# Performance work log

Measured on AMD Instinct MI355X. Metric: run time of the kernel, lower is better.

Reference implementation:

```python
import jax, jax.numpy as jnp
import numpy as np
import math

B, T, D, H, L = 64, 255, 512, 8, 8
CODEBOOK = 512
V = CODEBOOK + 3  # bos/eos/pad
COND_DIM = 512
MAX_LEN = 256
HD = D // H


def _layernorm(x, g, b, eps=1e-5):
    mu = jnp.mean(x, axis=-1, keepdims=True)
    var = jnp.mean(jnp.square(x - mu), axis=-1, keepdims=True)
    return (x - mu) * jax.lax.rsqrt(var + eps) * g + b


def setup_inputs() -> dict:
    key = jax.random.key(0)
    ks = jax.random.split(key, 24)
    s = 0.02
    d = {
        'tokens': jax.random.randint(ks[0], (B, T), 0, V),
        'cond': jax.random.normal(ks[1], (B, COND_DIM), jnp.float32),
        'emb': jax.random.normal(ks[2], (V, D), jnp.float32) * s,  # tied token_emb / head weight
        'pos_emb': jax.random.normal(ks[3], (1, MAX_LEN, D), jnp.float32) * s,
        'cond_w1': jax.random.normal(ks[4], (COND_DIM, D), jnp.float32) * s,
        'cond_b1': jnp.zeros((D,), jnp.float32),
        'cond_w2': jax.random.normal(ks[5], (D, D), jnp.float32) * s,
        'cond_b2': jnp.zeros((D,), jnp.float32),
        'ln1_g': jnp.ones((L, D), jnp.float32),
        'ln1_b': jnp.zeros((L, D), jnp.float32),
        'qkv_w': jax.random.normal(ks[6], (L, D, 3 * D), jnp.float32) * s,
        'qkv_b': jnp.zeros((L, 3 * D), jnp.float32),
        'proj_w': jax.random.normal(ks[7], (L, D, D), jnp.float32) * s,
        'proj_b': jnp.zeros((L, D), jnp.float32),
        'ln2_g': jnp.ones((L, D), jnp.float32),
        'ln2_b': jnp.zeros((L, D), jnp.float32),
        'mlp_w1': jax.random.normal(ks[8], (L, D, 4 * D), jnp.float32) * s,
        'mlp_b1': jnp.zeros((L, 4 * D), jnp.float32),
        'mlp_w2': jax.random.normal(ks[9], (L, 4 * D, D), jnp.float32) * s,
        'mlp_b2': jnp.zeros((L, D), jnp.float32),
        'lnf_g': jnp.ones((D,), jnp.float32),
        'lnf_b': jnp.zeros((D,), jnp.float32),
    }
    return d


def reference(tokens, cond, emb, pos_emb, cond_w1, cond_b1, cond_w2, cond_b2,
              ln1_g, ln1_b, qkv_w, qkv_b, proj_w, proj_b,
              ln2_g, ln2_b, mlp_w1, mlp_b1, mlp_w2, mlp_b2, lnf_g, lnf_b):
    b, t = tokens.shape
    h = emb[tokens] + pos_emb[:, :t, :]                              # [B,T,D]
    c = jax.nn.silu(cond @ cond_w1 + cond_b1) @ cond_w2 + cond_b2    # [B,D]
    h = jnp.concatenate([c[:, None, :], h], axis=1)                  # [B,S,D]
    S = t + 1
    causal = jnp.tril(jnp.ones((S, S), bool))
    scale = 1.0 / math.sqrt(HD)
    for i in range(L):
        x = _layernorm(h, ln1_g[i], ln1_b[i])
        qkv = (x @ qkv_w[i] + qkv_b[i]).reshape(b, S, 3, H, HD).transpose(2, 0, 3, 1, 4)
        q, k, v = qkv[0], qkv[1], qkv[2]                             # [B,H,S,hd]
        a = jnp.einsum('bhsd,bhtd->bhst', q, k) * scale
        a = jnp.where(causal, a, -jnp.inf)
        a = jax.nn.softmax(a, axis=-1)
        o = jnp.einsum('bhst,bhtd->bhsd', a, v).transpose(0, 2, 1, 3).reshape(b, S, D)
        h = h + o @ proj_w[i] + proj_b[i]
        x = _layernorm(h, ln2_g[i], ln2_b[i])
        h = h + jax.nn.gelu(x @ mlp_w1[i] + mlp_b1[i], approximate=False) @ mlp_w2[i] + mlp_b2[i]
    h = _layernorm(h, lnf_g, lnf_b)
    return (h @ emb.T)[:, 1:, :]                                     # [B,T,V]
```

## Files before the change

kernel.cpp:

```cpp
#include <hip/hip_runtime.h>
#include <hip/hip_bf16.h>

typedef __attribute__((ext_vector_type(8))) short bf16x8;
typedef __attribute__((ext_vector_type(4))) float f32x4;
typedef __attribute__((ext_vector_type(4))) unsigned short u16x4;
typedef __attribute__((ext_vector_type(8))) unsigned short u16x8;
typedef unsigned short u16;

#define DEV static __device__ __forceinline__

DEV float bf2f(u16 u) {
  union { unsigned int i; float f; } c; c.i = ((unsigned int)u) << 16; return c.f;
}
DEV u16 f2bf(float f) {
  union { float f; unsigned int i; } c; c.f = f;
  unsigned int i = c.i;
  i += 0x7FFFu + ((i >> 16) & 1u);
  return (u16)(i >> 16);
}

DEV void gload_lds16(const void* g, void* l) {
  __builtin_amdgcn_global_load_lds((const __attribute__((address_space(1))) void*)g,
                                   (__attribute__((address_space(3))) void*)l, 16, 0, 0);
}

DEV f32x4 mfma16(bf16x8 a, bf16x8 b, f32x4 c) {
  return __builtin_amdgcn_mfma_f32_16x16x32_bf16(a, b, c, 0, 0, 0);
}

__global__ __launch_bounds__(256) void ktranspose(const float* __restrict__ in, u16* __restrict__ out,
                                                  int K, int N) {
  __shared__ u16 tile[32][33];
  const float* src = in + (size_t)blockIdx.z * K * N;
  u16* dst = out + (size_t)blockIdx.z * K * N;
  const int n0 = blockIdx.x * 32, k0 = blockIdx.y * 32;
  const int tx = threadIdx.x, ty = threadIdx.y;
#pragma unroll
  for (int i = ty; i < 32; i += 8) tile[i][tx] = f2bf(src[(size_t)(k0 + i) * N + n0 + tx]);
  __syncthreads();
#pragma unroll
  for (int i = ty; i < 32; i += 8) dst[(size_t)(n0 + i) * K + k0 + tx] = tile[tx][i];
}

__global__ __launch_bounds__(256) void kcvt(const float* __restrict__ in, u16* __restrict__ out, int n) {
  int i = blockIdx.x * 256 + threadIdx.x;
  if (i < n) out[i] = f2bf(in[i]);
}

__global__ __launch_bounds__(256) void kcond(const float* __restrict__ cond, const float* __restrict__ w1,
                                             const float* __restrict__ b1, const float* __restrict__ w2,
                                             const float* __restrict__ b2, float* __restrict__ h) {
  __shared__ float xr[512];
  __shared__ float t1[512];
  const int b = blockIdx.x, tid = threadIdx.x;
  for (int i = tid; i < 512; i += 256) xr[i] = cond[b * 512 + i];
  __syncthreads();
  for (int j = tid; j < 512; j += 256) {
    float acc = b1[j];
    for (int k = 0; k < 512; ++k) acc += xr[k] * w1[k * 512 + j];
    t1[j] = acc / (1.f + __expf(-acc));
  }
  __syncthreads();
  for (int j = tid; j < 512; j += 256) {
    float acc = b2[j];
    for (int k = 0; k < 512; ++k) acc += t1[k] * w2[k * 512 + j];
    h[(size_t)b * 256 * 512 + j] = acc;
  }
}

__global__ __launch_bounds__(256) void kembed(const int* __restrict__ tok, const float* __restrict__ emb,
                                              const float* __restrict__ pos, float* __restrict__ h) {
  const int idx = blockIdx.x;
  const int b = idx / 255, t = idx % 255;
  const int c = threadIdx.x * 2;
  const int tk = tok[idx];
  float2 ev = *(const float2*)(emb + (size_t)tk * 512 + c);
  float2 pv = *(const float2*)(pos + (size_t)t * 512 + c);
  float2 r;
  r.x = ev.x + pv.x;
  r.y = ev.y + pv.y;
  *(float2*)(h + ((size_t)b * 256 + 1 + t) * 512 + c) = r;
}

__global__ __launch_bounds__(64) void kln(const float* __restrict__ hin, const float* __restrict__ g,
                                          const float* __restrict__ bt, u16* __restrict__ out) {
  const int row = blockIdx.x, lane = threadIdx.x;
  const float4* x = (const float4*)(hin + (size_t)row * 512);
  float4 v0 = x[lane], v1 = x[lane + 64];
  float s1 = v0.x + v0.y + v0.z + v0.w + v1.x + v1.y + v1.z + v1.w;
  float s2 = v0.x * v0.x + v0.y * v0.y + v0.z * v0.z + v0.w * v0.w +
             v1.x * v1.x + v1.y * v1.y + v1.z * v1.z + v1.w * v1.w;
#pragma unroll
  for (int off = 1; off < 64; off <<= 1) { s1 += __shfl_xor(s1, off); s2 += __shfl_xor(s2, off); }
  float mu = s1 * (1.f / 512.f);
  float var = s2 * (1.f / 512.f) - mu * mu;
  float rs = rsqrtf(var + 1e-5f);
  const int c0 = lane * 4;
  float4 g0 = *(const float4*)(g + c0), g1 = *(const float4*)(g + 256 + c0);
  float4 b0 = *(const float4*)(bt + c0), b1 = *(const float4*)(bt + 256 + c0);
  u16x4 o0, o1;
  o0[0] = f2bf((v0.x - mu) * rs * g0.x + b0.x);
  o0[1] = f2bf((v0.y - mu) * rs * g0.y + b0.y);
  o0[2] = f2bf((v0.z - mu) * rs * g0.z + b0.z);
  o0[3] = f2bf((v0.w - mu) * rs * g0.w + b0.w);
  o1[0] = f2bf((v1.x - mu) * rs * g1.x + b1.x);
  o1[1] = f2bf((v1.y - mu) * rs * g1.y + b1.y);
  o1[2] = f2bf((v1.z - mu) * rs * g1.z + b1.z);
  o1[3] = f2bf((v1.w - mu) * rs * g1.w + b1.w);
  *(u16x4*)(out + (size_t)row * 512 + c0) = o0;
  *(u16x4*)(out + (size_t)row * 512 + 256 + c0) = o1;
}

template<int MODE>
__global__ __launch_bounds__(256, 2) void kgemm(const u16* __restrict__ A, const u16* __restrict__ Bt,
                                                const float* __restrict__ bias, void* __restrict__ Cout,
                                                int M, int N, int K) {
  __shared__ __align__(16) u16 As[2][4096];
  __shared__ __align__(16) u16 Bs[2][4096];
  const int tid = threadIdx.x;
  const int lane = tid & 63;
  const int wr = tid >> 7, wc = (tid >> 6) & 1;
  const int m0 = blockIdx.x * 128, n0 = blockIdx.y * 128;
  const int nkt = K >> 5;
  const int Kb = K * 2;

  const int c0 = tid * 16;
  const int ar0 = c0 >> 6, ao0 = c0 & 63;
  const int ar1 = (c0 + 4096) >> 6, ao1 = (c0 + 4096) & 63;
  int br0 = n0 + ar0, br1 = n0 + ar1;
  if (MODE == 3) { br0 = min(br0, N - 1); br1 = min(br1, N - 1); }
  const char* Ab = (const char*)A;
  const char* Bb = (const char*)Bt;
  const size_t a0 = (size_t)(m0 + ar0) * Kb + ao0;
  const size_t a1 = (size_t)(m0 + ar1) * Kb + ao1;
  const size_t b0 = (size_t)br0 * Kb + ao0;
  const size_t b1 = (size_t)br1 * Kb + ao1;

  f32x4 acc[4][4];
#pragma unroll
  for (int i = 0; i < 4; ++i)
#pragma unroll
    for (int j = 0; j < 4; ++j) acc[i][j] = f32x4{0.f, 0.f, 0.f, 0.f};

  gload_lds16(Ab + a0, (char*)As[0] + c0);
  gload_lds16(Ab + a1, (char*)As[0] + c0 + 4096);
  gload_lds16(Bb + b0, (char*)Bs[0] + c0);
  gload_lds16(Bb + b1, (char*)Bs[0] + c0 + 4096);
  __syncthreads();

  const int aoff = (wr * 64 + (lane & 15)) * 32 + (lane >> 4) * 8;
  const int boff = (wc * 64 + (lane & 15)) * 32 + (lane >> 4) * 8;

  int buf = 0;
  for (int kt = 0; kt < nkt; ++kt) {
    if (kt + 1 < nkt) {
      const size_t ko = (size_t)(kt + 1) * 64;
      gload_lds16(Ab + a0 + ko, (char*)As[buf ^ 1] + c0);
      gload_lds16(Ab + a1 + ko, (char*)As[buf ^ 1] + c0 + 4096);
      gload_lds16(Bb + b0 + ko, (char*)Bs[buf ^ 1] + c0);
      gload_lds16(Bb + b1 + ko, (char*)Bs[buf ^ 1] + c0 + 4096);
    }
    bf16x8 aF[4], bF[4];
#pragma unroll
    for (int mt = 0; mt < 4; ++mt) aF[mt] = *(const bf16x8*)&As[buf][aoff + mt * 512];
#pragma unroll
    for (int nt = 0; nt < 4; ++nt) bF[nt] = *(const bf16x8*)&Bs[buf][boff + nt * 512];
#pragma unroll
    for (int mt = 0; mt < 4; ++mt)
#pragma unroll
      for (int nt = 0; nt < 4; ++nt)
        acc[mt][nt] = mfma16(aF[mt], bF[nt], acc[mt][nt]);
    __syncthreads();
    buf ^= 1;
  }

  float bv[4];
#pragma unroll
  for (int nt = 0; nt < 4; ++nt) {
    int col = n0 + wc * 64 + nt * 16 + (lane & 15);
    bv[nt] = (MODE == 3) ? 0.f : bias[col];
  }

  if (MODE == 0 || MODE == 1) {
    u16* C = (u16*)Cout;
#pragma unroll
    for (int mt = 0; mt < 4; ++mt)
#pragma unroll
      for (int r = 0; r < 4; ++r) {
        int row = m0 + wr * 64 + mt * 16 + (lane >> 4) * 4 + r;
        u16* cp = C + (size_t)row * N + n0 + wc * 64 + (lane & 15);
#pragma unroll
        for (int nt = 0; nt < 4; ++nt) {
          float v = acc[mt][nt][r] + bv[nt];
          if (MODE == 1) v = 0.5f * v * (1.f + erff(v * 0.70710678118f));
          cp[nt * 16] = f2bf(v);
        }
      }
  } else if (MODE == 2) {
    float* hC = (float*)Cout;
#pragma unroll
    for (int mt = 0; mt < 4; ++mt)
#pragma unroll
      for (int r = 0; r < 4; ++r) {
        int row = m0 + wr * 64 + mt * 16 + (lane >> 4) * 4 + r;
        float* hp = hC + (size_t)row * N + n0 + wc * 64 + (lane & 15);
#pragma unroll
        for (int nt = 0; nt < 4; ++nt) hp[nt * 16] += acc[mt][nt][r] + bv[nt];
      }
  } else {
    float* C = (float*)Cout;
#pragma unroll
    for (int mt = 0; mt < 4; ++mt)
#pragma unroll
      for (int r = 0; r < 4; ++r) {
        int row = m0 + wr * 64 + mt * 16 + (lane >> 4) * 4 + r;
        int s = row & 255;
        if (s == 0) continue;
        int bb = row >> 8;
        float* cp = C + ((size_t)bb * 255 + (s - 1)) * 515 + n0 + wc * 64 + (lane & 15);
#pragma unroll
        for (int nt = 0; nt < 4; ++nt) {
          int col = n0 + wc * 64 + nt * 16 + (lane & 15);
          if (col < 515) cp[nt * 16] = acc[mt][nt][r];
        }
      }
  }
}

__global__ __launch_bounds__(256, 1) void kattn(const u16* __restrict__ qkv, u16* __restrict__ o) {
  __shared__ __align__(16) u16 Ks[256][72];
  __shared__ __align__(16) u16 Vt[64][264];
  __shared__ __align__(16) u16 Ps[4][64][72];
  const int tid = threadIdx.x, wv = tid >> 6, lane = tid & 63;
  const int bh = blockIdx.x, bb = bh >> 3, hh = bh & 7;
  const size_t base = (size_t)bb * 256 * 1536 + hh * 64;

  for (int c = tid; c < 2048; c += 256) {
    int s = c >> 3, pp = c & 7;
    u16x8 kv = *(const u16x8*)(qkv + base + (size_t)s * 1536 + 512 + pp * 8);
    *(u16x8*)&Ks[s][pp * 8] = kv;
    u16x8 vv = *(const u16x8*)(qkv + base + (size_t)s * 1536 + 1024 + pp * 8);
#pragma unroll
    for (int j = 0; j < 8; ++j) Vt[pp * 8 + j][s] = vv[j];
  }
  __syncthreads();

  bf16x8 qf[4][2];
#pragma unroll
  for (int mt = 0; mt < 4; ++mt)
#pragma unroll
    for (int ks = 0; ks < 2; ++ks)
      qf[mt][ks] = *(const bf16x8*)(qkv + base +
                   (size_t)(wv * 64 + mt * 16 + (lane & 15)) * 1536 + ks * 32 + (lane >> 4) * 8);

  const float scale = 0.125f;
  float mrow[4][4], lsum[4][4];
#pragma unroll
  for (int mt = 0; mt < 4; ++mt)
#pragma unroll
    for (int r = 0; r < 4; ++r) { mrow[mt][r] = -1e30f; lsum[mt][r] = 0.f; }

  for (int ct = 0; ct <= wv; ++ct) {
    f32x4 sacc[4][4];
#pragma unroll
    for (int i = 0; i < 4; ++i)
#pragma unroll
      for (int j = 0; j < 4; ++j) sacc[i][j] = f32x4{0.f, 0.f, 0.f, 0.f};
#pragma unroll
    for (int ks = 0; ks < 2; ++ks) {
      bf16x8 kf[4];
#pragma unroll
      for (int nt = 0; nt < 4; ++nt)
        kf[nt] = *(const bf16x8*)&Ks[ct * 64 + nt * 16 + (lane & 15)][ks * 32 + (lane >> 4) * 8];
#pragma unroll
      for (int mt = 0; mt < 4; ++mt)
#pragma unroll
        for (int nt = 0; nt < 4; ++nt)
          sacc[mt][nt] = mfma16(qf[mt][ks], kf[nt], sacc[mt][nt]);
    }
#pragma unroll
    for (int mt = 0; mt < 4; ++mt)
#pragma unroll
      for (int r = 0; r < 4; ++r) {
        int srow = wv * 64 + mt * 16 + (lane >> 4) * 4 + r;
        float mx = -1e30f;
#pragma unroll
        for (int nt = 0; nt < 4; ++nt) {
          int tcol = ct * 64 + nt * 16 + (lane & 15);
          float v = sacc[mt][nt][r] * scale;
          if (tcol > srow) v = -1e30f;
          mx = fmaxf(mx, v);
        }
#pragma unroll
        for (int off = 1; off < 16; off <<= 1) mx = fmaxf(mx, __shfl_xor(mx, off));
        mrow[mt][r] = fmaxf(mrow[mt][r], mx);
      }
  }

  f32x4 oacc[4][4];
#pragma unroll
  for (int i = 0; i < 4; ++i)
#pragma unroll
    for (int j = 0; j < 4; ++j) oacc[i][j] = f32x4{0.f, 0.f, 0.f, 0.f};

  for (int ct = 0; ct <= wv; ++ct) {
    f32x4 sacc[4][4];
#pragma unroll
    for (int i = 0; i < 4; ++i)
#pragma unroll
      for (int j = 0; j < 4; ++j) sacc[i][j] = f32x4{0.f, 0.f, 0.f, 0.f};
#pragma unroll
    for (int ks = 0; ks < 2; ++ks) {
      bf16x8 kf[4];
#pragma unroll
      for (int nt = 0; nt < 4; ++nt)
        kf[nt] = *(const bf16x8*)&Ks[ct * 64 + nt * 16 + (lane & 15)][ks * 32 + (lane >> 4) * 8];
#pragma unroll
      for (int mt = 0; mt < 4; ++mt)
#pragma unroll
        for (int nt = 0; nt < 4; ++nt)
          sacc[mt][nt] = mfma16(qf[mt][ks], kf[nt], sacc[mt][nt]);
    }
#pragma unroll
    for (int mt = 0; mt < 4; ++mt)
#pragma unroll
      for (int r = 0; r < 4; ++r) {
        int srow = wv * 64 + mt * 16 + (lane >> 4) * 4 + r;
        float ps = 0.f;
#pragma unroll
        for (int nt = 0; nt < 4; ++nt) {
          int tcol = ct * 64 + nt * 16 + (lane & 15);
          float v = sacc[mt][nt][r] * scale;
          float pe = (tcol > srow) ? 0.f : __expf(v - mrow[mt][r]);
          ps += pe;
          Ps[wv][mt * 16 + (lane >> 4) * 4 + r][nt * 16 + (lane & 15)] = f2bf(pe);
        }
#pragma unroll
        for (int off = 1; off < 16; off <<= 1) ps += __shfl_xor(ps, off);
        lsum[mt][r] += ps;
      }
#pragma unroll
    for (int ks = 0; ks < 2; ++ks) {
      bf16x8 pf[4], vf[4];
#pragma unroll
      for (int mt = 0; mt < 4; ++mt)
        pf[mt] = *(const bf16x8*)&Ps[wv][mt * 16 + (lane & 15)][ks * 32 + (lane >> 4) * 8];
#pragma unroll
      for (int nt = 0; nt < 4; ++nt)
        vf[nt] = *(const bf16x8*)&Vt[nt * 16 + (lane & 15)][ct * 64 + ks * 32 + (lane >> 4) * 8];
#pragma unroll
      for (int mt = 0; mt < 4; ++mt)
#pragma unroll
        for (int nt = 0; nt < 4; ++nt)
          oacc[mt][nt] = mfma16(pf[mt], vf[nt], oacc[mt][nt]);
    }
  }

#pragma unroll
  for (int mt = 0; mt < 4; ++mt)
#pragma unroll
    for (int r = 0; r < 4; ++r) {
      int s = wv * 64 + mt * 16 + (lane >> 4) * 4 + r;
      float inv = 1.f / lsum[mt][r];
      u16* op = o + ((size_t)bb * 256 + s) * 512 + hh * 64 + (lane & 15);
#pragma unroll
      for (int nt = 0; nt < 4; ++nt) op[nt * 16] = f2bf(oacc[mt][nt][r] * inv);
    }
}

extern "C" void kernel_launch(void* const* d_in, const int* in_sizes, int n_in,
                              void* d_out, int out_size, void* d_ws, size_t ws_size,
                              hipStream_t stream) {
  const int* tokens = (const int*)d_in[0];
  const float* cond = (const float*)d_in[1];
  const float* emb = (const float*)d_in[2];
  const float* pos = (const float*)d_in[3];
  const float* cw1 = (const float*)d_in[4];
  const float* cb1 = (const float*)d_in[5];
  const float* cw2 = (const float*)d_in[6];
  const float* cb2 = (const float*)d_in[7];
  const float* ln1g = (const float*)d_in[8];
  const float* ln1b = (const float*)d_in[9];
  const float* qkvw = (const float*)d_in[10];
  const float* qkvb = (const float*)d_in[11];
  const float* projw = (const float*)d_in[12];
  const float* projb = (const float*)d_in[13];
  const float* ln2g = (const float*)d_in[14];
  const float* ln2b = (const float*)d_in[15];
  const float* w1 = (const float*)d_in[16];
  const float* b1 = (const float*)d_in[17];
  const float* w2 = (const float*)d_in[18];
  const float* b2 = (const float*)d_in[19];
  const float* lnfg = (const float*)d_in[20];
  const float* lnfb = (const float*)d_in[21];

  const size_t NEEDED = (size_t)16384 * 512 * 4
                      + (size_t)16384 * 512 * 2
                      + (size_t)16384 * 2048 * 2
                      + (size_t)8 * 1536 * 512 * 2
                      + (size_t)8 * 512 * 512 * 2
                      + (size_t)8 * 2048 * 512 * 2
                      + (size_t)8 * 512 * 2048 * 2;
  if (ws_size < NEEDED) return;

  char* p = (char*)d_ws;
  float* h = (float*)p;        p += (size_t)16384 * 512 * 4;
  u16* xln = (u16*)p;          p += (size_t)16384 * 512 * 2;
  u16* big = (u16*)p;          p += (size_t)16384 * 2048 * 2;
  u16* attn_o = big + (size_t)16384 * 1536;
  u16* embB = big;
  u16* qkvT = (u16*)p;         p += (size_t)8 * 1536 * 512 * 2;
  u16* projT = (u16*)p;        p += (size_t)8 * 512 * 512 * 2;
  u16* w1T = (u16*)p;          p += (size_t)8 * 2048 * 512 * 2;
  u16* w2T = (u16*)p;          p += (size_t)8 * 512 * 2048 * 2;

  ktranspose<<<dim3(48, 16, 8), dim3(32, 8), 0, stream>>>(qkvw, qkvT, 512, 1536);
  ktranspose<<<dim3(16, 16, 8), dim3(32, 8), 0, stream>>>(projw, projT, 512, 512);
  ktranspose<<<dim3(64, 16, 8), dim3(32, 8), 0, stream>>>(w1, w1T, 512, 2048);
  ktranspose<<<dim3(16, 64, 8), dim3(32, 8), 0, stream>>>(w2, w2T, 2048, 512);

  kembed<<<16320, 256, 0, stream>>>(tokens, emb, pos, h);
  kcond<<<64, 256, 0, stream>>>(cond, cw1, cb1, cw2, cb2, h);

  for (int l = 0; l < 8; ++l) {
    kln<<<16384, 64, 0, stream>>>(h, ln1g + l * 512, ln1b + l * 512, xln);
    kgemm<0><<<dim3(128, 12), 256, 0, stream>>>(xln, qkvT + (size_t)l * 1536 * 512,
                                                qkvb + l * 1536, big, 16384, 1536, 512);
    kattn<<<512, 256, 0, stream>>>(big, attn_o);
    kgemm<2><<<dim3(128, 4), 256, 0, stream>>>(attn_o, projT + (size_t)l * 512 * 512,
                                               projb + l * 512, h, 16384, 512, 512);
    kln<<<16384, 64, 0, stream>>>(h, ln2g + l * 512, ln2b + l * 512, xln);
    kgemm<1><<<dim3(128, 16), 256, 0, stream>>>(xln, w1T + (size_t)l * 2048 * 512,
                                                b1 + l * 2048, big, 16384, 2048, 512);
    kgemm<2><<<dim3(128, 4), 256, 0, stream>>>(big, w2T + (size_t)l * 512 * 2048,
                                               b2 + l * 512, h, 16384, 512, 2048);
  }
  kln<<<16384, 64, 0, stream>>>(h, lnfg, lnfb, xln);
  kcvt<<<1030, 256, 0, stream>>>(emb, embB, 515 * 512);
  kgemm<3><<<dim3(128, 5), 256, 0, stream>>>(xln, embB, nullptr, d_out, 16384, 515, 512);
}
```

Before: 2.018 ms.

## Use 256x256 swizzled-LDS GEMM for QKV/MLP1, fast erf GELU, 4-row LN blocks

```diff
diff --git a/kernel.cpp b/kernel.cpp
--- a/kernel.cpp
+++ b/kernel.cpp
@@ -27,6 +27,16 @@
 DEV f32x4 mfma16(bf16x8 a, bf16x8 b, f32x4 c) {
   return __builtin_amdgcn_mfma_f32_16x16x32_bf16(a, b, c, 0, 0, 0);
 }
+
+DEV float fasterf(float x) {
+  float ax = fabsf(x);
+  float t = 1.0f / (1.0f + 0.3275911f * ax);
+  float y = t * (0.254829592f + t * (-0.284496736f + t * (1.421413741f +
+            t * (-1.453152027f + t * 1.061405429f))));
+  float r = 1.0f - y * __expf(-ax * ax);
+  return copysignf(r, x);
+}
+DEV float gelu(float v) { return 0.5f * v * (1.0f + fasterf(v * 0.70710678118f)); }
 
 __global__ __launch_bounds__(256) void ktranspose(const float* __restrict__ in, u16* __restrict__ out,
                                                   int K, int N) {
@@ -82,9 +92,9 @@
   *(float2*)(h + ((size_t)b * 256 + 1 + t) * 512 + c) = r;
 }
 
-__global__ __launch_bounds__(64) void kln(const float* __restrict__ hin, const float* __restrict__ g,
-                                          const float* __restrict__ bt, u16* __restrict__ out) {
-  const int row = blockIdx.x, lane = threadIdx.x;
+__global__ __launch_bounds__(256) void kln(const float* __restrict__ hin, const float* __restrict__ g,
+                                           const float* __restrict__ bt, u16* __restrict__ out) {
+  const int row = blockIdx.x * 4 + (threadIdx.x >> 6), lane = threadIdx.x & 63;
   const float4* x = (const float4*)(hin + (size_t)row * 512);
   float4 v0 = x[lane], v1 = x[lane + 64];
   float s1 = v0.x + v0.y + v0.z + v0.w + v1.x + v1.y + v1.z + v1.w;
@@ -112,6 +122,108 @@
 }
 
 template<int MODE>
+__global__ __launch_bounds__(512, 2) void kgemm256(const u16* __restrict__ A, const u16* __restrict__ Bt,
+                                                   const float* __restrict__ bias, u16* __restrict__ C,
+                                                   int M, int N, int K) {
+  __shared__ __align__(16) u16 As[2][16384];
+  __shared__ __align__(16) u16 Bs[2][16384];
+  const int tid = threadIdx.x;
+  const int lane = tid & 63;
+  const int wid = tid >> 6;
+  const int wr = wid >> 2;
+  const int wc = wid & 3;
+  const int m0 = blockIdx.x * 256, n0 = blockIdx.y * 256;
+  const int NKT = K >> 6;
+  const size_t Kb = (size_t)K * 2;
+
+  size_t asrc[4], bsrc[4];
+  int dsto[4];
+#pragma unroll
+  for (int j = 0; j < 4; ++j) {
+    int d = j * 8192 + tid * 16;
+    int row = d >> 7;
+    int col = (d & 127) ^ ((row & 7) << 4);
+    asrc[j] = (size_t)(m0 + row) * Kb + col;
+    bsrc[j] = (size_t)(n0 + row) * Kb + col;
+    dsto[j] = d;
+  }
+  const char* Ab = (const char*)A;
+  const char* Bb = (const char*)Bt;
+
+  f32x4 acc[8][4];
+#pragma unroll
+  for (int i = 0; i < 8; ++i)
+#pragma unroll
+    for (int j = 0; j < 4; ++j) acc[i][j] = f32x4{0.f, 0.f, 0.f, 0.f};
+
+#pragma unroll
+  for (int j = 0; j < 4; ++j) {
+    gload_lds16(Ab + asrc[j], (char*)As[0] + dsto[j]);
+    gload_lds16(Bb + bsrc[j], (char*)Bs[0] + dsto[j]);
+  }
+  asm volatile("s_waitcnt vmcnt(0)" ::: "memory");
+  __builtin_amdgcn_s_barrier();
+  __builtin_amdgcn_sched_barrier(0);
+
+  const int aswz = (lane & 7) << 4;
+  const int arow = wr * 128 + (lane & 15);
+  const int brow = wc * 64 + (lane & 15);
+  const int kchunk = (lane >> 4) * 16;
+
+  for (int kt = 0; kt < NKT; ++kt) {
+    const int buf = kt & 1;
+    if (kt + 1 < NKT) {
+      const size_t ko = (size_t)(kt + 1) * 128;
+#pragma unroll
+      for (int j = 0; j < 4; ++j) {
+        gload_lds16(Ab + asrc[j] + ko, (char*)As[buf ^ 1] + dsto[j]);
+        gload_lds16(Bb + bsrc[j] + ko, (char*)Bs[buf ^ 1] + dsto[j]);
+      }
+    }
+    const char* Ap = (const char*)As[buf];
+    const char* Bp = (const char*)Bs[buf];
+    bf16x8 bF[4][2];
+#pragma unroll
+    for (int n = 0; n < 4; ++n)
+#pragma unroll
+      for (int ks = 0; ks < 2; ++ks)
+        bF[n][ks] = *(const bf16x8*)(Bp + (brow + n * 16) * 128 + ((ks * 64 + kchunk) ^ aswz));
+#pragma unroll
+    for (int m = 0; m < 8; ++m) {
+      const char* rp = Ap + (arow + m * 16) * 128;
+      bf16x8 a0 = *(const bf16x8*)(rp + (kchunk ^ aswz));
+      bf16x8 a1 = *(const bf16x8*)(rp + ((64 + kchunk) ^ aswz));
+#pragma unroll
+      for (int n = 0; n < 4; ++n) {
+        acc[m][n] = mfma16(a0, bF[n][0], acc[m][n]);
+        acc[m][n] = mfma16(a1, bF[n][1], acc[m][n]);
+      }
+    }
+    asm volatile("s_waitcnt vmcnt(0)" ::: "memory");
+    __builtin_amdgcn_s_barrier();
+    __builtin_amdgcn_sched_barrier(0);
+  }
+
+  float bv[4];
+#pragma unroll
+  for (int n = 0; n < 4; ++n) bv[n] = bias[n0 + wc * 64 + n * 16 + (lane & 15)];
+
+#pragma unroll
+  for (int m = 0; m < 8; ++m)
+#pragma unroll
+    for (int r = 0; r < 4; ++r) {
+      int row = m0 + wr * 128 + m * 16 + (lane >> 4) * 4 + r;
+      u16* cp = C + (size_t)row * N + n0 + wc * 64 + (lane & 15);
+#pragma unroll
+      for (int n = 0; n < 4; ++n) {
+        float v = acc[m][n][r] + bv[n];
+        if (MODE == 1) v = gelu(v);
+        cp[n * 16] = f2bf(v);
+      }
+    }
+}
+
+template<int MODE>
 __global__ __launch_bounds__(256, 2) void kgemm(const u16* __restrict__ A, const u16* __restrict__ Bt,
                                                 const float* __restrict__ bias, void* __restrict__ Cout,
                                                 int M, int N, int K) {
@@ -181,22 +293,7 @@
     bv[nt] = (MODE == 3) ? 0.f : bias[col];
   }
 
-  if (MODE == 0 || MODE == 1) {
-    u16* C = (u16*)Cout;
-#pragma unroll
-    for (int mt = 0; mt < 4; ++mt)
-#pragma unroll
-      for (int r = 0; r < 4; ++r) {
-        int row = m0 + wr * 64 + mt * 16 + (lane >> 4) * 4 + r;
-        u16* cp = C + (size_t)row * N + n0 + wc * 64 + (lane & 15);
-#pragma unroll
-        for (int nt = 0; nt < 4; ++nt) {
-          float v = acc[mt][nt][r] + bv[nt];
-          if (MODE == 1) v = 0.5f * v * (1.f + erff(v * 0.70710678118f));
-          cp[nt * 16] = f2bf(v);
-        }
-      }
-  } else if (MODE == 2) {
+  if (MODE == 2) {
     float* hC = (float*)Cout;
 #pragma unroll
     for (int mt = 0; mt < 4; ++mt)
@@ -423,19 +520,19 @@
   kcond<<<64, 256, 0, stream>>>(cond, cw1, cb1, cw2, cb2, h);
 
   for (int l = 0; l < 8; ++l) {
-    kln<<<16384, 64, 0, stream>>>(h, ln1g + l * 512, ln1b + l * 512, xln);
-    kgemm<0><<<dim3(128, 12), 256, 0, stream>>>(xln, qkvT + (size_t)l * 1536 * 512,
-                                                qkvb + l * 1536, big, 16384, 1536, 512);
+    kln<<<4096, 256, 0, stream>>>(h, ln1g + l * 512, ln1b + l * 512, xln);
+    kgemm256<0><<<dim3(64, 6), 512, 0, stream>>>(xln, qkvT + (size_t)l * 1536 * 512,
+                                                 qkvb + l * 1536, big, 16384, 1536, 512);
     kattn<<<512, 256, 0, stream>>>(big, attn_o);
     kgemm<2><<<dim3(128, 4), 256, 0, stream>>>(attn_o, projT + (size_t)l * 512 * 512,
                                                projb + l * 512, h, 16384, 512, 512);
-    kln<<<16384, 64, 0, stream>>>(h, ln2g + l * 512, ln2b + l * 512, xln);
-    kgemm<1><<<dim3(128, 16), 256, 0, stream>>>(xln, w1T + (size_t)l * 2048 * 512,
-                                                b1 + l * 2048, big, 16384, 2048, 512);
+    kln<<<4096, 256, 0, stream>>>(h, ln2g + l * 512, ln2b + l * 512, xln);
+    kgemm256<1><<<dim3(64, 8), 512, 0, stream>>>(xln, w1T + (size_t)l * 2048 * 512,
+                                                 b1 + l * 2048, big, 16384, 2048, 512);
     kgemm<2><<<dim3(128, 4), 256, 0, stream>>>(big, w2T + (size_t)l * 512 * 2048,
                                                b2 + l * 512, h, 16384, 512, 2048);
   }
-  kln<<<16384, 64, 0, stream>>>(h, lnfg, lnfb, xln);
+  kln<<<4096, 256, 0, stream>>>(h, lnfg, lnfb, xln);
   kcvt<<<1030, 256, 0, stream>>>(emb, embB, 515 * 512);
   kgemm<3><<<dim3(128, 5), 256, 0, stream>>>(xln, embB, nullptr, d_out, 16384, 515, 512);
 }
```

Result: slower. 2.078 ms (+3.0%).
